# Kernel optimization log

Measured on AMD Instinct MI355X. Metric: run time of the kernel, lower is better.

## Reference

```python
import math
import jax, jax.numpy as jnp
import numpy as np

F, B, J, D, H = 120, 64, 22, 512, 4  # frames, batch, joints, d_model, heads
DFF = 2048
EPS = 1e-6


def setup_inputs() -> dict:
    key = jax.random.key(0)
    ks = jax.random.split(key, 32)
    w = lambda k, s: jax.random.normal(k, s, jnp.float32) * 0.02
    inp = {
        "x": jax.random.normal(ks[0], (F, B, J, D), jnp.float32),
        "timesteps_embs": jax.random.normal(ks[1], (1, B, D), jnp.float32),
        "spat_mask": jnp.ones((1, 1, 1, 1, 1), jnp.int32),
        "temp_mask": jnp.ones((1, 1, 1, 1, 1), jnp.int32),
        "layer_ind": 1,
    }
    i = 2
    for p in ("s", "t"):  # spatial / temporal attention params
        for m in ("q", "k", "v", "o"):
            inp[p + "W" + m] = w(ks[i], (D, D)); i += 1
            inp[p + "b" + m] = w(ks[i], (D,)); i += 1
    inp["ffW1"] = w(ks[i], (D, DFF)); inp["ffb1"] = w(ks[i + 1], (DFF,))
    inp["ffW2"] = w(ks[i + 2], (DFF, D)); inp["ffb2"] = w(ks[i + 3], (D,))
    for n in ("n1", "n2", "n3"):
        inp[n + "a"] = jnp.ones((D,), jnp.float32)
        inp[n + "b"] = jnp.zeros((D,), jnp.float32)
    return inp


def _norm(x, a, b):
    # custom Norm: uses torch.std (ddof=1) and eps added to std (not var)
    mu = jnp.mean(x, axis=-1, keepdims=True)
    sd = jnp.std(x, axis=-1, ddof=1, keepdims=True)
    return a * (x - mu) / (sd + EPS) + b


def _mha(x, Wq, bq, Wk, bk, Wv, bv, Wo, bo, h, mask):
    d1, bs, d2, dm = x.shape
    dk = dm // h
    split = lambda t: (t.reshape(d1, bs, d2, h, dk)).transpose(0, 1, 3, 2, 4)  # (d1,bs,h,d2,dk)
    q = split(x @ Wq + bq)
    k = split(x @ Wk + bk)
    v = split(x @ Wv + bv)
    scores = jnp.einsum("fbhqd,fbhkd->fbhqk", q, k) / math.sqrt(dk)
    m = jnp.swapaxes(mask, 0, 1).astype(jnp.float32)  # mask.transpose(0,1).float()
    scores = jnp.where(m == 0, -1e9, scores)
    p = jax.nn.softmax(scores, axis=-1)
    o = jnp.einsum("fbhqk,fbhkd->fbhqd", p, v)
    o = o.transpose(0, 1, 3, 2, 4).reshape(d1, bs, d2, dm)
    return o @ Wo + bo


def _forward(x, timesteps_embs,
             sWq, sbq, sWk, sbk, sWv, sbv, sWo, sbo,
             tWq, tbq, tWk, tbk, tWv, tbv, tWo, tbo,
             ffW1, ffb1, ffW2, ffb2,
             n1a, n1b, n2a, n2b, n3a, n3b,
             spat_mask, temp_mask):
    # layer_ind > 0 path: no positional-encoding additions (eval mode: dropout = identity)
    f, bs, nj, dm = x.shape
    ts = jnp.broadcast_to(timesteps_embs[:, :, None, :], (f, bs, 1, dm))
    x1 = jnp.concatenate([ts, x], axis=2)                      # (F,B,J+1,D)
    x1 = x + _mha(x1, sWq, sbq, sWk, sbk, sWv, sbv, sWo, sbo, H, spat_mask)[:, :, 1:, :]
    x1 = jnp.swapaxes(_norm(x1, n1a, n1b), 0, 2)               # (J,B,F,D)
    ts2 = jnp.broadcast_to(timesteps_embs[:, :, None, :], (x1.shape[0], bs, 1, dm))
    x2 = jnp.concatenate([ts2, x1], axis=2)                    # (J,B,F+1,D)
    x2 = x1 + _mha(x2, tWq, tbq, tWk, tbk, tWv, tbv, tWo, tbo, H, temp_mask)[:, :, 1:, :]
    x2 = jnp.swapaxes(_norm(x2, n2a, n2b), 0, 2)               # (F,B,J,D)
    ff = jax.nn.gelu(x2 @ ffW1 + ffb1, approximate=False) @ ffW2 + ffb2
    return _norm(x2 + ff, n3a, n3b)


def reference(x, timesteps_embs,
              sWq, sbq, sWk, sbk, sWv, sbv, sWo, sbo,
              tWq, tbq, tWk, tbk, tWv, tbv, tWo, tbo,
              ffW1, ffb1, ffW2, ffb2,
              n1a, n1b, n2a, n2b, n3a, n3b,
              spat_mask, temp_mask, layer_ind):
    # layer_ind is fixed to 1 (layer_ind==0 branch is unreachable/broken in source)
    return _forward(x, timesteps_embs,
                    sWq, sbq, sWk, sbk, sWv, sbv, sWo, sbo,
                    tWq, tbq, tWk, tbk, tWv, tbv, tWo, tbo,
                    ffW1, ffb1, ffW2, ffb2,
                    n1a, n1b, n2a, n2b, n3a, n3b,
                    spat_mask, temp_mask)
```

## Files before the change

kernel.cpp:

```cpp
#include <hip/hip_runtime.h>
#include <hip/hip_bf16.h>
#include <math.h>


#define F_DIM 120
#define B_DIM 64
#define J_DIM 22
#define H_DIM 4
#define M_TOK (F_DIM * B_DIM * J_DIM)

#define DEV static __device__ __forceinline__

typedef short bf16x8 __attribute__((ext_vector_type(8)));
typedef short us8 __attribute__((ext_vector_type(8)));
typedef float f32x4 __attribute__((ext_vector_type(4)));

struct __align__(8) us4 { unsigned short x, y, z, w; };

DEV unsigned short f2b(float f) {
  unsigned u = __float_as_uint(f);
  u += 0x7fffu + ((u >> 16) & 1u);
  return (unsigned short)(u >> 16);
}
DEV float b2f(unsigned short u) { return __uint_as_float(((unsigned)u) << 16); }

#define GLOAD16(g, l)                                                          \
  __builtin_amdgcn_global_load_lds(                                            \
      (const __attribute__((address_space(1))) void*)(g),                      \
      (__attribute__((address_space(3))) void*)(l), 16, 0, 0)

enum { EPI_QKV = 0, EPI_GELU = 1, EPI_RES = 2, EPI_ACC = 3, EPI_RESB = 4,
       EPI_ROB = 5,
       EPI_RBB = 6 };

__global__ __launch_bounds__(256)
void cast_k(const float* __restrict__ in, unsigned short* __restrict__ out, int n8) {
  for (int i = blockIdx.x * 256 + threadIdx.x; i < n8; i += gridDim.x * 256) {
    const float4 a = ((const float4*)in)[i * 2];
    const float4 b = ((const float4*)in)[i * 2 + 1];
    us8 v;
    v[0] = f2b(a.x); v[1] = f2b(a.y); v[2] = f2b(a.z); v[3] = f2b(a.w);
    v[4] = f2b(b.x); v[5] = f2b(b.y); v[6] = f2b(b.z); v[7] = f2b(b.w);
    *(us8*)&out[i * 8] = v;
  }
}

__global__ __launch_bounds__(256)
void tcast_k(const float* __restrict__ W, unsigned short* __restrict__ WT, int K, int N) {
  __shared__ float t[32][33];
  const int n0 = blockIdx.x * 32, k0 = blockIdx.y * 32;
  const int tx = threadIdx.x, ty = threadIdx.y;
#pragma unroll
  for (int i = 0; i < 4; ++i)
    t[ty + i * 8][tx] = W[(size_t)(k0 + ty + i * 8) * N + n0 + tx];
  __syncthreads();
#pragma unroll
  for (int i = 0; i < 4; ++i)
    WT[(size_t)(n0 + ty + i * 8) * K + k0 + tx] = f2b(t[tx][ty + i * 8]);
}

__global__ __launch_bounds__(256)
void tsproj_k(const float* __restrict__ ts, const float* __restrict__ W,
              const float* __restrict__ bias, unsigned short* __restrict__ out) {
  __shared__ float tsr[512];
  const int b = blockIdx.x, tid = threadIdx.x;
  for (int i = tid; i < 512; i += 256) tsr[i] = ts[b * 512 + i];
  __syncthreads();
  const int n0 = tid, n1 = tid + 256;
  float a0 = bias[n0], a1 = bias[n1];
  for (int k = 0; k < 512; ++k) {
    const float t = tsr[k];
    a0 += t * W[(size_t)k * 512 + n0];
    a1 += t * W[(size_t)k * 512 + n1];
  }
  out[b * 512 + n0] = f2b(a0);
  out[b * 512 + n1] = f2b(a1);
}

template<int EPI>
DEV void epi_store(float v, int row, int col, const float* b0, const float* b1,
                   const float* b2, const void* res, float* outF,
                   unsigned short* o0, unsigned short* o1, unsigned short* o2,
                   int ldo, float scale) {
  if constexpr (EPI == EPI_QKV) {
    const int seg = col >> 9;
    const int cl = col & 511;
    const float* bs = (seg == 0) ? b0 : (seg == 1) ? b1 : b2;
    unsigned short* ob = (seg == 0) ? o0 : (seg == 1) ? o1 : o2;
    const float sc = (seg == 0) ? scale : 1.f;
    v = (v + bs[cl]) * sc;
    ob[(size_t)row * 512 + cl] = f2b(v);
  } else if constexpr (EPI == EPI_GELU) {
    v += b0[col];
    const float a2 = 1.5957691216057308f * (v + 0.044715f * v * v * v);
    const float g = v / (1.f + __expf(-a2));
    o0[(size_t)row * ldo + col] = f2b(g);
  } else if constexpr (EPI == EPI_RES) {
    const size_t off = (size_t)row * 512 + col;
    outF[off] = v + b0[col] + ((const float*)res)[off];
  } else if constexpr (EPI == EPI_RESB) {
    const size_t off = (size_t)row * 512 + col;
    outF[off] = v + b0[col] + b2f(((const unsigned short*)res)[off]);
  } else if constexpr (EPI == EPI_ROB) {
    const size_t off = (size_t)row * 512 + col;
    o0[off] = f2b(v + b0[col] + ((const float*)res)[off]);
  } else if constexpr (EPI == EPI_RBB) {
    const size_t off = (size_t)row * 512 + col;
    o0[off] = f2b(v + b0[col] + b2f(((const unsigned short*)res)[off]));
  } else {
    const size_t off = (size_t)row * 512 + col;
    outF[off] = v + outF[off];
  }
}

template<int EPI>
__global__ __launch_bounds__(512, 4)
void gemm256_k(const unsigned short* __restrict__ Ab, const unsigned short* __restrict__ Wt,
               const float* __restrict__ b0, const float* __restrict__ b1, const float* __restrict__ b2,
               const void* __restrict__ res, float* __restrict__ outF,
               unsigned short* __restrict__ o0, unsigned short* __restrict__ o1, unsigned short* __restrict__ o2,
               int lda, int ldw, int ldo, int nk, int nx, float scale) {
  __shared__ unsigned short As[3][8192];
  __shared__ unsigned short Bs[3][4096];
  const int tid = threadIdx.x;
  const int chunkg = gridDim.x >> 3;
  const int wg = (blockIdx.x & 7) * chunkg + (blockIdx.x >> 3);
  const int nbase = (wg % nx) * 128;
  const int mbase = (wg / nx) * 256;
  const int lane = tid & 63;
  const int w = tid >> 6;
  const int wr = (w >> 1) * 64;
  const int wc = (w & 1) * 64;
  const int l15 = lane & 15;
  const int lhi = lane >> 4;

  const int crow = lane >> 2;
  const int ccol = (((lane & 3) ^ ((lane >> 3) & 3)) << 3);
  const unsigned short* gA0 = Ab + (size_t)(mbase + 32 * w + crow) * lda + ccol;
  const unsigned short* gA1 = gA0 + (size_t)16 * lda;
  const unsigned short* gB0 = Wt + (size_t)(nbase + 16 * w + crow) * ldw + ccol;

  auto stage = [&](int bb, int kt) {
    GLOAD16(gA0 + kt, &As[bb][(2 * w) * 512]);
    GLOAD16(gA1 + kt, &As[bb][(2 * w + 1) * 512]);
    GLOAD16(gB0 + kt, &Bs[bb][w * 512]);
  };

  f32x4 acc[4][4] = {};
  const int KT = nk >> 5;
  const int swz = ((lhi ^ ((l15 >> 1) & 3)) << 3);

  stage(0, 0);
  stage(1, 32);
  asm volatile("s_waitcnt vmcnt(3)" ::: "memory");
  __builtin_amdgcn_s_barrier();

  for (int t = 0; t < KT; ++t) {
    const unsigned short* as = As[t % 3];
    const unsigned short* bs = Bs[t % 3];
    if (t + 2 < KT) stage((t + 2) % 3, (t + 2) << 5);
    bf16x8 afr[4], bfr[4];
#pragma unroll
    for (int i = 0; i < 4; ++i) afr[i] = *(const bf16x8*)&as[(wr + i * 16 + l15) * 32 + swz];
#pragma unroll
    for (int j = 0; j < 4; ++j) bfr[j] = *(const bf16x8*)&bs[(wc + j * 16 + l15) * 32 + swz];
#pragma unroll
    for (int i = 0; i < 4; ++i)
#pragma unroll
      for (int j = 0; j < 4; ++j)
        acc[i][j] = __builtin_amdgcn_mfma_f32_16x16x32_bf16(afr[i], bfr[j], acc[i][j], 0, 0, 0);
    if (t + 2 < KT)      asm volatile("s_waitcnt vmcnt(3) lgkmcnt(0)" ::: "memory");
    else if (t + 1 < KT) asm volatile("s_waitcnt vmcnt(0) lgkmcnt(0)" ::: "memory");
    else                 asm volatile("s_waitcnt lgkmcnt(0)" ::: "memory");
    __builtin_amdgcn_s_barrier();
  }

#pragma unroll
  for (int i = 0; i < 4; ++i)
#pragma unroll
    for (int j = 0; j < 4; ++j) {
      const int row0 = mbase + wr + i * 16 + (lhi << 2);
      const int col = nbase + wc + j * 16 + l15;
#pragma unroll
      for (int q = 0; q < 4; ++q)
        epi_store<EPI>(acc[i][j][q], row0 + q, col, b0, b1, b2, res, outF, o0, o1, o2, ldo, scale);
    }
}

template<int EPI>
__global__ __launch_bounds__(256)
void gemm_k(const unsigned short* __restrict__ Ab, const unsigned short* __restrict__ Wt,
            const float* __restrict__ b0, const float* __restrict__ b1, const float* __restrict__ b2,
            const void* __restrict__ res, float* __restrict__ outF,
            unsigned short* __restrict__ o0, unsigned short* __restrict__ o1, unsigned short* __restrict__ o2,
            int lda, int ldw, int ldo, int nk, int nx, float scale) {
  __shared__ unsigned short As[3][4096];
  __shared__ unsigned short Bs[3][4096];
  const int tid = threadIdx.x;
  const int chunkg = gridDim.x >> 3;
  const int wg = (blockIdx.x & 7) * chunkg + (blockIdx.x >> 3);
  const int nbase = (wg % nx) * 128;
  const int mbase = (wg / nx) * 128;
  const int lane = tid & 63;
  const int w = tid >> 6;
  const int wr = (w >> 1) * 64;
  const int wc = (w & 1) * 64;
  const int l15 = lane & 15;
  const int lhi = lane >> 4;

  const int crow = lane >> 2;
  const int ccol = (((lane & 3) ^ ((lane >> 3) & 3)) << 3);
  const unsigned short* gA0 = Ab + (size_t)(mbase + 32 * w + crow) * lda + ccol;
  const unsigned short* gA1 = gA0 + (size_t)16 * lda;
  const unsigned short* gB0 = Wt + (size_t)(nbase + 32 * w + crow) * ldw + ccol;
  const unsigned short* gB1 = gB0 + (size_t)16 * ldw;

  auto stage = [&](int bb, int kt) {
    GLOAD16(gA0 + kt, &As[bb][(2 * w) * 512]);
    GLOAD16(gA1 + kt, &As[bb][(2 * w + 1) * 512]);
    GLOAD16(gB0 + kt, &Bs[bb][(2 * w) * 512]);
    GLOAD16(gB1 + kt, &Bs[bb][(2 * w + 1) * 512]);
  };

  f32x4 acc[4][4] = {};
  const int KT = nk >> 5;
  const int swz = ((lhi ^ ((l15 >> 1) & 3)) << 3);

  stage(0, 0);
  stage(1, 32);
  asm volatile("s_waitcnt vmcnt(4)" ::: "memory");
  __builtin_amdgcn_s_barrier();

  for (int t = 0; t < KT; ++t) {
    const unsigned short* as = As[t % 3];
    const unsigned short* bs = Bs[t % 3];
    if (t + 2 < KT) stage((t + 2) % 3, (t + 2) << 5);
    bf16x8 afr[4], bfr[4];
#pragma unroll
    for (int i = 0; i < 4; ++i) afr[i] = *(const bf16x8*)&as[(wr + i * 16 + l15) * 32 + swz];
#pragma unroll
    for (int j = 0; j < 4; ++j) bfr[j] = *(const bf16x8*)&bs[(wc + j * 16 + l15) * 32 + swz];
#pragma unroll
    for (int i = 0; i < 4; ++i)
#pragma unroll
      for (int j = 0; j < 4; ++j)
        acc[i][j] = __builtin_amdgcn_mfma_f32_16x16x32_bf16(afr[i], bfr[j], acc[i][j], 0, 0, 0);
    if (t + 2 < KT)      asm volatile("s_waitcnt vmcnt(4) lgkmcnt(0)" ::: "memory");
    else if (t + 1 < KT) asm volatile("s_waitcnt vmcnt(0) lgkmcnt(0)" ::: "memory");
    else                 asm volatile("s_waitcnt lgkmcnt(0)" ::: "memory");
    __builtin_amdgcn_s_barrier();
  }

#pragma unroll
  for (int i = 0; i < 4; ++i)
#pragma unroll
    for (int j = 0; j < 4; ++j) {
      const int row0 = mbase + wr + i * 16 + (lhi << 2);
      const int col = nbase + wc + j * 16 + l15;
#pragma unroll
      for (int q = 0; q < 4; ++q)
        epi_store<EPI>(acc[i][j][q], row0 + q, col, b0, b1, b2, res, outF, o0, o1, o2, ldo, scale);
    }
}

template<int EPI>
__global__ __launch_bounds__(256)
void gemmf_k(const float* __restrict__ Af, const unsigned short* __restrict__ Wt,
             const float* __restrict__ b0, const float* __restrict__ b1, const float* __restrict__ b2,
             const void* __restrict__ res, float* __restrict__ outF,
             unsigned short* __restrict__ o0, unsigned short* __restrict__ o1, unsigned short* __restrict__ o2,
             int lda, int ldw, int ldo, int nk, int nx, float scale) {
  __shared__ unsigned short As[128][40];
  __shared__ unsigned short Bs[128][40];
  const int tid = threadIdx.x;
  const int chunkg = gridDim.x >> 3;
  const int wg = (blockIdx.x & 7) * chunkg + (blockIdx.x >> 3);
  const int nbase = (wg % nx) * 128;
  const int mbase = (wg / nx) * 128;
  const int lane = tid & 63;
  const int w = tid >> 6;
  const int wr = (w >> 1) * 64;
  const int wc = (w & 1) * 64;
  const int l15 = lane & 15;
  const int lhi = lane >> 4;

  float4 ra[4];
  us4 rb[4];
  auto loadAB = [&](int kt) {
#pragma unroll
    for (int i = 0; i < 4; ++i) {
      const int g = i * 256 + tid;
      const int r = g >> 3;
      const int c = (g & 7) << 2;
      ra[i] = *(const float4*)(Af + (size_t)(mbase + r) * lda + kt + c);
      rb[i] = *(const us4*)(Wt + (size_t)(nbase + r) * ldw + kt + c);
    }
  };
  auto storeAB = [&]() {
#pragma unroll
    for (int i = 0; i < 4; ++i) {
      const int g = i * 256 + tid;
      const int r = g >> 3;
      const int c = (g & 7) << 2;
      us4 ua;
      ua.x = f2b(ra[i].x); ua.y = f2b(ra[i].y); ua.z = f2b(ra[i].z); ua.w = f2b(ra[i].w);
      *(us4*)&As[r][c] = ua;
      *(us4*)&Bs[r][c] = rb[i];
    }
  };

  f32x4 acc[4][4] = {};
  const int KT = nk >> 5;
  loadAB(0);
  storeAB();
  __syncthreads();
  for (int t = 0; t < KT; ++t) {
    if (t + 1 < KT) loadAB((t + 1) << 5);
    bf16x8 afr[4], bfr[4];
    const int klo = lhi << 3;
#pragma unroll
    for (int i = 0; i < 4; ++i) afr[i] = *(const bf16x8*)&As[wr + i * 16 + l15][klo];
#pragma unroll
    for (int j = 0; j < 4; ++j) bfr[j] = *(const bf16x8*)&Bs[wc + j * 16 + l15][klo];
#pragma unroll
    for (int i = 0; i < 4; ++i)
#pragma unroll
      for (int j = 0; j < 4; ++j)
        acc[i][j] = __builtin_amdgcn_mfma_f32_16x16x32_bf16(afr[i], bfr[j], acc[i][j], 0, 0, 0);
    __syncthreads();
    if (t + 1 < KT) { storeAB(); __syncthreads(); }
  }

#pragma unroll
  for (int i = 0; i < 4; ++i)
#pragma unroll
    for (int j = 0; j < 4; ++j) {
      const int row0 = mbase + wr + i * 16 + (lhi << 2);
      const int col = nbase + wc + j * 16 + l15;
#pragma unroll
      for (int q = 0; q < 4; ++q)
        epi_store<EPI>(acc[i][j][q], row0 + q, col, b0, b1, b2, res, outF, o0, o1, o2, ldo, scale);
    }
}

__global__ __launch_bounds__(256)
void attn_t_k(const unsigned short* __restrict__ Qb, const unsigned short* __restrict__ Kb,
              const unsigned short* __restrict__ Vb, const unsigned short* __restrict__ kts,
              const unsigned short* __restrict__ vts, unsigned short* __restrict__ Ob) {
  __shared__ unsigned short Ps[128][134];
  __shared__ unsigned short Vt[64][134];
  const int tid = threadIdx.x;
  const int inst = blockIdx.x >> 2;
  const int h = blockIdx.x & 3;
  const int b = inst & (B_DIM - 1);
  const size_t rowbase = (size_t)inst * 120;
  const int hoff = h * 128;
  const int lane = tid & 63;
  const int w = tid >> 6;
  const int wr = w * 32;
  const int l15 = lane & 15;
  const int lhi = lane >> 4;

  auto stageV = [&](int half) {
    for (int e = tid; e < 2048; e += 256) {
      const int d4 = (e & 15) << 2;
      const int key = e >> 4;
      us4 v;
      if (key <= 120) {
        const unsigned short* src = (key == 0) ? (vts + b * 512) : (Vb + (rowbase + key - 1) * 512);
        v = *(const us4*)(src + hoff + half * 64 + d4);
      } else { v.x = 0; v.y = 0; v.z = 0; v.w = 0; }
      Vt[d4 + 0][key] = v.x; Vt[d4 + 1][key] = v.y; Vt[d4 + 2][key] = v.z; Vt[d4 + 3][key] = v.w;
    }
  };
  stageV(0);

  bf16x8 qa[2][4];
#pragma unroll
  for (int i = 0; i < 2; ++i) {
    const int row = min(wr + i * 16 + l15, 119);
    const unsigned short* qp = Qb + (rowbase + row) * 512 + hoff;
#pragma unroll
    for (int kt = 0; kt < 4; ++kt)
      qa[i][kt] = *(const bf16x8*)(qp + kt * 32 + lhi * 8);
  }

  f32x4 acc[2][8] = {};
#pragma unroll
  for (int kt = 0; kt < 4; ++kt) {
    const int klo = kt * 32 + lhi * 8;
    bf16x8 kb[8];
#pragma unroll
    for (int j = 0; j < 8; ++j) {
      const int key = min(j * 16 + l15, 120);
      const unsigned short* kp = (key == 0) ? (kts + b * 512) : (Kb + (rowbase + key - 1) * 512);
      kb[j] = *(const bf16x8*)(kp + hoff + klo);
    }
#pragma unroll
    for (int i = 0; i < 2; ++i)
#pragma unroll
      for (int j = 0; j < 8; ++j)
        acc[i][j] = __builtin_amdgcn_mfma_f32_16x16x32_bf16(qa[i][kt], kb[j], acc[i][j], 0, 0, 0);
  }

  float rinv[2][4];
#pragma unroll
  for (int i = 0; i < 2; ++i)
#pragma unroll
    for (int q = 0; q < 4; ++q) {
      float m = -1e30f;
#pragma unroll
      for (int j = 0; j < 8; ++j)
        if (j * 16 + l15 <= 120) m = fmaxf(m, acc[i][j][q]);
#pragma unroll
      for (int mk = 1; mk < 16; mk <<= 1) m = fmaxf(m, __shfl_xor(m, mk, 64));
      float s = 0.f;
#pragma unroll
      for (int j = 0; j < 8; ++j) {
        const float e = (j * 16 + l15 <= 120) ? __expf(acc[i][j][q] - m) : 0.f;
        acc[i][j][q] = e; s += e;
      }
#pragma unroll
      for (int mk = 1; mk < 16; mk <<= 1) s += __shfl_xor(s, mk, 64);
      rinv[i][q] = 1.f / s;
    }

#pragma unroll
  for (int i = 0; i < 2; ++i)
#pragma unroll
    for (int j = 0; j < 8; ++j)
#pragma unroll
      for (int q = 0; q < 4; ++q)
        Ps[wr + i * 16 + lhi * 4 + q][j * 16 + l15] = f2b(acc[i][j][q]);

  __syncthreads();

#pragma unroll
  for (int half = 0; half < 2; ++half) {
    if (half == 1) {
      __syncthreads();
      stageV(1);
      __syncthreads();
    }
    f32x4 oac[2][4] = {};
#pragma unroll
    for (int kt = 0; kt < 4; ++kt) {
      const int klo = kt * 32 + lhi * 8;
      bf16x8 pa[2], vb[4];
#pragma unroll
      for (int i = 0; i < 2; ++i) pa[i] = *(const bf16x8*)&Ps[wr + i * 16 + l15][klo];
#pragma unroll
      for (int jd = 0; jd < 4; ++jd) vb[jd] = *(const bf16x8*)&Vt[jd * 16 + l15][klo];
#pragma unroll
      for (int i = 0; i < 2; ++i)
#pragma unroll
        for (int jd = 0; jd < 4; ++jd)
          oac[i][jd] = __builtin_amdgcn_mfma_f32_16x16x32_bf16(pa[i], vb[jd], oac[i][jd], 0, 0, 0);
    }
#pragma unroll
    for (int i = 0; i < 2; ++i)
#pragma unroll
      for (int q = 0; q < 4; ++q) {
        const int r = wr + i * 16 + lhi * 4 + q;
        if (r < 120) {
          const float sc = rinv[i][q];
#pragma unroll
          for (int jd = 0; jd < 4; ++jd)
            Ob[(rowbase + r) * 512 + hoff + half * 64 + jd * 16 + l15] = f2b(oac[i][jd][q] * sc);
        }
      }
  }
}

__global__ __launch_bounds__(256)
void attn_s_k(const unsigned short* __restrict__ Qb, const unsigned short* __restrict__ Kb,
              const unsigned short* __restrict__ Vb, const unsigned short* __restrict__ kts,
              const unsigned short* __restrict__ vts, unsigned short* __restrict__ Ob) {
  __shared__ unsigned short Ps[4][32][34];
  __shared__ unsigned short Vt[4][128][34];
  const int tid = threadIdx.x;
  const int inst = blockIdx.x;
  const int b = inst & (B_DIM - 1);
  const size_t rowbase = (size_t)inst * 22;
  const int lane = tid & 63;
  const int h = tid >> 6;
  const int l15 = lane & 15;
  const int lhi = lane >> 4;
  const int hoff = h * 128;

  for (int e = tid; e < 4096; e += 256) {
    const int h2 = e >> 10;
    const int rem = e & 1023;
    const int key = rem >> 5;
    const int d4 = (rem & 31) << 2;
    us4 v;
    if (key <= 22) {
      const unsigned short* src = (key == 0) ? (vts + b * 512) : (Vb + (rowbase + key - 1) * 512);
      v = *(const us4*)(src + h2 * 128 + d4);
    } else { v.x = 0; v.y = 0; v.z = 0; v.w = 0; }
    Vt[h2][d4 + 0][key] = v.x; Vt[h2][d4 + 1][key] = v.y; Vt[h2][d4 + 2][key] = v.z; Vt[h2][d4 + 3][key] = v.w;
  }

  bf16x8 qa[2][4];
#pragma unroll
  for (int i = 0; i < 2; ++i) {
    const int row = min(i * 16 + l15, 21);
    const unsigned short* qp = Qb + (rowbase + row) * 512 + hoff;
#pragma unroll
    for (int kt = 0; kt < 4; ++kt)
      qa[i][kt] = *(const bf16x8*)(qp + kt * 32 + lhi * 8);
  }

  f32x4 acc[2][2] = {};
#pragma unroll
  for (int kt = 0; kt < 4; ++kt) {
    const int klo = kt * 32 + lhi * 8;
    bf16x8 kb[2];
#pragma unroll
    for (int j = 0; j < 2; ++j) {
      const int key = min(j * 16 + l15, 22);
      const unsigned short* kp = (key == 0) ? (kts + b * 512) : (Kb + (rowbase + key - 1) * 512);
      kb[j] = *(const bf16x8*)(kp + hoff + klo);
    }
#pragma unroll
    for (int i = 0; i < 2; ++i)
#pragma unroll
      for (int j = 0; j < 2; ++j)
        acc[i][j] = __builtin_amdgcn_mfma_f32_16x16x32_bf16(qa[i][kt], kb[j], acc[i][j], 0, 0, 0);
  }

  float rinv[2][4];
#pragma unroll
  for (int i = 0; i < 2; ++i)
#pragma unroll
    for (int q = 0; q < 4; ++q) {
      float m = -1e30f;
#pragma unroll
      for (int j = 0; j < 2; ++j)
        if (j * 16 + l15 <= 22) m = fmaxf(m, acc[i][j][q]);
#pragma unroll
      for (int mk = 1; mk < 16; mk <<= 1) m = fmaxf(m, __shfl_xor(m, mk, 64));
      float s = 0.f;
#pragma unroll
      for (int j = 0; j < 2; ++j) {
        const float e = (j * 16 + l15 <= 22) ? __expf(acc[i][j][q] - m) : 0.f;
        acc[i][j][q] = e; s += e;
      }
#pragma unroll
      for (int mk = 1; mk < 16; mk <<= 1) s += __shfl_xor(s, mk, 64);
      rinv[i][q] = 1.f / s;
    }

#pragma unroll
  for (int i = 0; i < 2; ++i)
#pragma unroll
    for (int j = 0; j < 2; ++j)
#pragma unroll
      for (int q = 0; q < 4; ++q)
        Ps[h][i * 16 + lhi * 4 + q][j * 16 + l15] = f2b(acc[i][j][q]);

  __syncthreads();

  f32x4 oac[2][8] = {};
  {
    const int klo = lhi * 8;
    bf16x8 pa[2];
#pragma unroll
    for (int i = 0; i < 2; ++i) pa[i] = *(const bf16x8*)&Ps[h][i * 16 + l15][klo];
#pragma unroll
    for (int jd = 0; jd < 8; ++jd) {
      const bf16x8 vb = *(const bf16x8*)&Vt[h][jd * 16 + l15][klo];
#pragma unroll
      for (int i = 0; i < 2; ++i)
        oac[i][jd] = __builtin_amdgcn_mfma_f32_16x16x32_bf16(pa[i], vb, oac[i][jd], 0, 0, 0);
    }
  }

#pragma unroll
  for (int i = 0; i < 2; ++i)
#pragma unroll
    for (int q = 0; q < 4; ++q) {
      const int r = i * 16 + lhi * 4 + q;
      if (r < 22) {
        const float sc = rinv[i][q];
#pragma unroll
        for (int jd = 0; jd < 8; ++jd)
          Ob[(rowbase + r) * 512 + hoff + jd * 16 + l15] = f2b(oac[i][jd][q] * sc);
      }
    }
}

__global__ __launch_bounds__(256)
void norm_k(const float* __restrict__ in, float* __restrict__ out,
            unsigned short* __restrict__ outB,
            const float* __restrict__ ga, const float* __restrict__ gb, const int mode) {
  const int r = blockIdx.x * 4 + (threadIdx.x >> 6);
  const int lane = threadIdx.x & 63;
  const float* row = in + (size_t)r * 512;
  const float4 v0 = *(const float4*)&row[lane * 4];
  const float4 v1 = *(const float4*)&row[256 + lane * 4];
  float s = v0.x + v0.y + v0.z + v0.w + v1.x + v1.y + v1.z + v1.w;
  float ss = v0.x * v0.x + v0.y * v0.y + v0.z * v0.z + v0.w * v0.w
           + v1.x * v1.x + v1.y * v1.y + v1.z * v1.z + v1.w * v1.w;
#pragma unroll
  for (int m = 1; m < 64; m <<= 1) { s += __shfl_xor(s, m, 64); ss += __shfl_xor(ss, m, 64); }
  const float mean = s * (1.f / 512.f);
  const float var = (ss - 512.f * mean * mean) * (1.f / 511.f);
  const float inv = 1.f / (sqrtf(fmaxf(var, 0.f)) + 1e-6f);
  int ro;
  if (mode == 0) ro = r;
  else if (mode == 1) {
    const int f = r / (B_DIM * J_DIM);
    const int bb = (r / J_DIM) % B_DIM;
    const int j = r % J_DIM;
    ro = (j * B_DIM + bb) * F_DIM + f;
  } else {
    const int j = r / (B_DIM * F_DIM);
    const int bb = (r / F_DIM) % B_DIM;
    const int f = r % F_DIM;
    ro = (f * B_DIM + bb) * J_DIM + j;
  }
  const float4 g0 = *(const float4*)&ga[lane * 4];
  const float4 g1 = *(const float4*)&ga[256 + lane * 4];
  const float4 h0 = *(const float4*)&gb[lane * 4];
  const float4 h1 = *(const float4*)&gb[256 + lane * 4];
  float4 y0, y1;
  y0.x = g0.x * (v0.x - mean) * inv + h0.x;
  y0.y = g0.y * (v0.y - mean) * inv + h0.y;
  y0.z = g0.z * (v0.z - mean) * inv + h0.z;
  y0.w = g0.w * (v0.w - mean) * inv + h0.w;
  y1.x = g1.x * (v1.x - mean) * inv + h1.x;
  y1.y = g1.y * (v1.y - mean) * inv + h1.y;
  y1.z = g1.z * (v1.z - mean) * inv + h1.z;
  y1.w = g1.w * (v1.w - mean) * inv + h1.w;
  if (out) {
    float* orow = out + (size_t)ro * 512;
    *(float4*)&orow[lane * 4] = y0;
    *(float4*)&orow[256 + lane * 4] = y1;
  }
  if (outB) {
    us4 a, b;
    a.x = f2b(y0.x); a.y = f2b(y0.y); a.z = f2b(y0.z); a.w = f2b(y0.w);
    b.x = f2b(y1.x); b.y = f2b(y1.y); b.z = f2b(y1.z); b.w = f2b(y1.w);
    *(us4*)&outB[(size_t)ro * 512 + lane * 4] = a;
    *(us4*)&outB[(size_t)ro * 512 + 256 + lane * 4] = b;
  }
}

__global__ __launch_bounds__(256)
void normb_k(const unsigned short* __restrict__ in, float* __restrict__ out,
             unsigned short* __restrict__ outB,
             const float* __restrict__ ga, const float* __restrict__ gb, const int mode) {
  const int r = blockIdx.x * 4 + (threadIdx.x >> 6);
  const int lane = threadIdx.x & 63;
  const us8 wv = *(const us8*)&in[(size_t)r * 512 + lane * 8];
  float v[8];
  float s = 0.f, ss = 0.f;
#pragma unroll
  for (int e = 0; e < 8; ++e) {
    v[e] = b2f((unsigned short)wv[e]);
    s += v[e]; ss += v[e] * v[e];
  }
#pragma unroll
  for (int m = 1; m < 64; m <<= 1) { s += __shfl_xor(s, m, 64); ss += __shfl_xor(ss, m, 64); }
  const float mean = s * (1.f / 512.f);
  const float var = (ss - 512.f * mean * mean) * (1.f / 511.f);
  const float inv = 1.f / (sqrtf(fmaxf(var, 0.f)) + 1e-6f);
  int ro;
  if (mode == 0) ro = r;
  else if (mode == 1) {
    const int f = r / (B_DIM * J_DIM);
    const int bb = (r / J_DIM) % B_DIM;
    const int j = r % J_DIM;
    ro = (j * B_DIM + bb) * F_DIM + f;
  } else {
    const int j = r / (B_DIM * F_DIM);
    const int bb = (r / F_DIM) % B_DIM;
    const int f = r % F_DIM;
    ro = (f * B_DIM + bb) * J_DIM + j;
  }
  const float4 g0 = *(const float4*)&ga[lane * 8];
  const float4 g1 = *(const float4*)&ga[lane * 8 + 4];
  const float4 h0 = *(const float4*)&gb[lane * 8];
  const float4 h1 = *(const float4*)&gb[lane * 8 + 4];
  float y[8];
  y[0] = g0.x * (v[0] - mean) * inv + h0.x;
  y[1] = g0.y * (v[1] - mean) * inv + h0.y;
  y[2] = g0.z * (v[2] - mean) * inv + h0.z;
  y[3] = g0.w * (v[3] - mean) * inv + h0.w;
  y[4] = g1.x * (v[4] - mean) * inv + h1.x;
  y[5] = g1.y * (v[5] - mean) * inv + h1.y;
  y[6] = g1.z * (v[6] - mean) * inv + h1.z;
  y[7] = g1.w * (v[7] - mean) * inv + h1.w;
  if (out) {
    float* orow = out + (size_t)ro * 512 + lane * 8;
    *(float4*)&orow[0] = *(float4*)&y[0];
    *(float4*)&orow[4] = *(float4*)&y[4];
  }
  if (outB) {
    us8 o;
#pragma unroll
    for (int e = 0; e < 8; ++e) o[e] = f2b(y[e]);
    *(us8*)&outB[(size_t)ro * 512 + lane * 8] = o;
  }
}

extern "C" void kernel_launch(void* const* d_in, const int* in_sizes, int n_in,
                              void* d_out, int out_size, void* d_ws, size_t ws_size,
                              hipStream_t stream) {
  const float* x   = (const float*)d_in[0];
  const float* tse = (const float*)d_in[1];
  const float* sWq = (const float*)d_in[5];  const float* sbq = (const float*)d_in[6];
  const float* sWk = (const float*)d_in[7];  const float* sbk = (const float*)d_in[8];
  const float* sWv = (const float*)d_in[9];  const float* sbv = (const float*)d_in[10];
  const float* sWo = (const float*)d_in[11]; const float* sbo = (const float*)d_in[12];
  const float* tWq = (const float*)d_in[13]; const float* tbq = (const float*)d_in[14];
  const float* tWk = (const float*)d_in[15]; const float* tbk = (const float*)d_in[16];
  const float* tWv = (const float*)d_in[17]; const float* tbv = (const float*)d_in[18];
  const float* tWo = (const float*)d_in[19]; const float* tbo = (const float*)d_in[20];
  const float* ffW1 = (const float*)d_in[21]; const float* ffb1 = (const float*)d_in[22];
  const float* ffW2 = (const float*)d_in[23]; const float* ffb2 = (const float*)d_in[24];
  const float* n1a = (const float*)d_in[25]; const float* n1b = (const float*)d_in[26];
  const float* n2a = (const float*)d_in[27]; const float* n2b = (const float*)d_in[28];
  const float* n3a = (const float*)d_in[29]; const float* n3b = (const float*)d_in[30];

  char* p = (char*)d_ws;
  auto carve = [&](size_t bytes) { void* r = (void*)p; p += (bytes + 255) & ~(size_t)255; return r; };

  unsigned short* sQKVt = (unsigned short*)carve((size_t)3 * 512 * 512 * 2);
  unsigned short* sOT   = (unsigned short*)carve((size_t)512 * 512 * 2);
  unsigned short* tQKVt = (unsigned short*)carve((size_t)3 * 512 * 512 * 2);
  unsigned short* tOT   = (unsigned short*)carve((size_t)512 * 512 * 2);
  unsigned short* W1T   = (unsigned short*)carve((size_t)2048 * 512 * 2);
  unsigned short* W2T   = (unsigned short*)carve((size_t)512 * 2048 * 2);
  unsigned short* ktss  = (unsigned short*)carve((size_t)64 * 512 * 2);
  unsigned short* vtss  = (unsigned short*)carve((size_t)64 * 512 * 2);
  unsigned short* ktst  = (unsigned short*)carve((size_t)64 * 512 * 2);
  unsigned short* vtst  = (unsigned short*)carve((size_t)64 * 512 * 2);
  unsigned short* Qb    = (unsigned short*)carve((size_t)M_TOK * 512 * 2);

  unsigned short* Kb = (unsigned short*)d_out;
  unsigned short* Vb = Kb + (size_t)M_TOK * 512;
  float* outF = (float*)d_out;

  const bool bigws = ws_size >= (size_t)873725952ull;
  float* Rbuf = nullptr;
  unsigned short* Hb  = nullptr;
  unsigned short* xb  = nullptr;
  unsigned short* rb1 = nullptr;
  if (bigws) {
    Hb = (unsigned short*)carve((size_t)M_TOK * 2048 * 2);
    xb = Hb;
    rb1 = Hb + (size_t)M_TOK * 512;
  } else {
    Rbuf = (float*)carve((size_t)M_TOK * 512 * 4);
  }

  const float QSCALE = 0.08838834764831845f;

  {
    dim3 tb(32, 8);
    tcast_k<<<dim3(16, 16), tb, 0, stream>>>(sWq, sQKVt, 512, 512);
    tcast_k<<<dim3(16, 16), tb, 0, stream>>>(sWk, sQKVt + 262144, 512, 512);
    tcast_k<<<dim3(16, 16), tb, 0, stream>>>(sWv, sQKVt + 524288, 512, 512);
    tcast_k<<<dim3(16, 16), tb, 0, stream>>>(sWo, sOT, 512, 512);
    tcast_k<<<dim3(16, 16), tb, 0, stream>>>(tWq, tQKVt, 512, 512);
    tcast_k<<<dim3(16, 16), tb, 0, stream>>>(tWk, tQKVt + 262144, 512, 512);
    tcast_k<<<dim3(16, 16), tb, 0, stream>>>(tWv, tQKVt + 524288, 512, 512);
    tcast_k<<<dim3(16, 16), tb, 0, stream>>>(tWo, tOT, 512, 512);
    tcast_k<<<dim3(64, 16), tb, 0, stream>>>(ffW1, W1T, 512, 2048);
    tcast_k<<<dim3(16, 64), tb, 0, stream>>>(ffW2, W2T, 2048, 512);
  }
  tsproj_k<<<B_DIM, 256, 0, stream>>>(tse, sWk, sbk, ktss);
  tsproj_k<<<B_DIM, 256, 0, stream>>>(tse, sWv, sbv, vtss);
  tsproj_k<<<B_DIM, 256, 0, stream>>>(tse, tWk, tbk, ktst);
  tsproj_k<<<B_DIM, 256, 0, stream>>>(tse, tWv, tbv, vtst);

  const int MT = M_TOK / 128;
  const int MT2 = M_TOK / 256;

  if (bigws) {
    cast_k<<<2048, 256, 0, stream>>>(x, xb, M_TOK * 512 / 8);
    gemm256_k<EPI_QKV><<<12 * MT2, 512, 0, stream>>>(
        xb, sQKVt, sbq, sbk, sbv, nullptr, nullptr, Qb, Kb, Vb, 512, 512, 512, 512, 12, QSCALE);
    attn_s_k<<<dim3(F_DIM * B_DIM), 256, 0, stream>>>(Qb, Kb, Vb, ktss, vtss, Qb);
    gemm256_k<EPI_ROB><<<4 * MT2, 512, 0, stream>>>(
        Qb, sOT, sbo, nullptr, nullptr, x, nullptr, Kb, nullptr, nullptr, 512, 512, 512, 512, 4, 1.f);
    normb_k<<<M_TOK / 4, 256, 0, stream>>>(Kb, nullptr, rb1, n1a, n1b, 1);

    gemm256_k<EPI_QKV><<<12 * MT2, 512, 0, stream>>>(
        rb1, tQKVt, tbq, tbk, tbv, nullptr, nullptr, Qb, Kb, Vb, 512, 512, 512, 512, 12, QSCALE);
    attn_t_k<<<dim3(J_DIM * B_DIM * H_DIM), 256, 0, stream>>>(Qb, Kb, Vb, ktst, vtst, Qb);
    gemm256_k<EPI_RBB><<<4 * MT2, 512, 0, stream>>>(
        Qb, tOT, tbo, nullptr, nullptr, rb1, nullptr, Kb, nullptr, nullptr, 512, 512, 512, 512, 4, 1.f);
    normb_k<<<M_TOK / 4, 256, 0, stream>>>(Kb, nullptr, Qb, n2a, n2b, 2);

    gemm256_k<EPI_GELU><<<16 * MT2, 512, 0, stream>>>(
        Qb, W1T, ffb1, nullptr, nullptr, nullptr, nullptr, Hb, nullptr, nullptr,
        512, 512, 2048, 512, 16, 1.f);
    gemm256_k<EPI_RBB><<<4 * MT2, 512, 0, stream>>>(
        Hb, W2T, ffb2, nullptr, nullptr, Qb, nullptr, Qb, nullptr, nullptr,
        2048, 2048, 512, 2048, 4, 1.f);
    normb_k<<<M_TOK / 4, 256, 0, stream>>>(Qb, outF, nullptr, n3a, n3b, 0);
  } else {
    gemmf_k<EPI_QKV><<<12 * MT, 256, 0, stream>>>(
        x, sQKVt, sbq, sbk, sbv, nullptr, nullptr, Qb, Kb, Vb, 512, 512, 512, 512, 12, QSCALE);
    attn_s_k<<<dim3(F_DIM * B_DIM), 256, 0, stream>>>(Qb, Kb, Vb, ktss, vtss, Qb);
    gemm_k<EPI_RES><<<4 * MT, 256, 0, stream>>>(
        Qb, sOT, sbo, nullptr, nullptr, x, outF, nullptr, nullptr, nullptr, 512, 512, 512, 512, 4, 1.f);
    norm_k<<<M_TOK / 4, 256, 0, stream>>>(outF, Rbuf, nullptr, n1a, n1b, 1);

    gemmf_k<EPI_QKV><<<12 * MT, 256, 0, stream>>>(
        Rbuf, tQKVt, tbq, tbk, tbv, nullptr, nullptr, Qb, Kb, Vb, 512, 512, 512, 512, 12, QSCALE);
    attn_t_k<<<dim3(J_DIM * B_DIM * H_DIM), 256, 0, stream>>>(Qb, Kb, Vb, ktst, vtst, Qb);
    gemm_k<EPI_RES><<<4 * MT, 256, 0, stream>>>(
        Qb, tOT, tbo, nullptr, nullptr, Rbuf, outF, nullptr, nullptr, nullptr, 512, 512, 512, 512, 4, 1.f);
    norm_k<<<M_TOK / 4, 256, 0, stream>>>(outF, Rbuf, Qb, n2a, n2b, 2);

    for (int c = 0; c < 4; ++c) {
      gemm_k<EPI_GELU><<<4 * MT, 256, 0, stream>>>(
          Qb, W1T + (size_t)c * 512 * 512, ffb1 + c * 512, nullptr, nullptr,
          nullptr, nullptr, Qb, nullptr, nullptr, 512, 512, 512, 512, 4, 1.f);
      if (c == 0)
        gemm_k<EPI_RES><<<4 * MT, 256, 0, stream>>>(
            Qb, W2T + c * 512, ffb2, nullptr, nullptr, Rbuf, outF,
            nullptr, nullptr, nullptr, 512, 2048, 512, 512, 4, 1.f);
      else
        gemm_k<EPI_ACC><<<4 * MT, 256, 0, stream>>>(
            Qb, W2T + c * 512, nullptr, nullptr, nullptr, nullptr, outF,
            nullptr, nullptr, nullptr, 512, 2048, 512, 512, 4, 1.f);
    }
    norm_k<<<M_TOK / 4, 256, 0, stream>>>(outF, outF, nullptr, n3a, n3b, 0);
  }
}
```

Baseline: 3.210 ms.

## Batch weight casts and ts projections into single launches; read bf16 residual

Merges the eight 512x512 weight transpose-cast launches into one 3D-grid kernel and the four timestep projection launches into one kernel. The projection kernel now splits K across four thread groups with a shared-memory reduction, giving it more parallelism. The spatial output-projection epilogue now reads the residual from the bf16 copy of x instead of the fp32 input, which cuts residual read bandwidth but rounds the residual to bf16. These setup kernels are small next to the GEMMs, so the overall effect is likely small.

```diff
diff --git a/kernel.cpp b/kernel.cpp
--- a/kernel.cpp
+++ b/kernel.cpp
@@ -59,22 +59,47 @@
     WT[(size_t)(n0 + ty + i * 8) * K + k0 + tx] = f2b(t[tx][ty + i * 8]);
 }
 
+struct Tc8Args { const float* W[8]; unsigned short* WT[8]; };
 __global__ __launch_bounds__(256)
-void tsproj_k(const float* __restrict__ ts, const float* __restrict__ W,
-              const float* __restrict__ bias, unsigned short* __restrict__ out) {
+void tcast8_k(Tc8Args a) {
+  __shared__ float t[32][33];
+  const float* W = a.W[blockIdx.z];
+  unsigned short* WT = a.WT[blockIdx.z];
+  const int n0 = blockIdx.x * 32, k0 = blockIdx.y * 32;
+  const int tx = threadIdx.x, ty = threadIdx.y;
+#pragma unroll
+  for (int i = 0; i < 4; ++i)
+    t[ty + i * 8][tx] = W[(size_t)(k0 + ty + i * 8) * 512 + n0 + tx];
+  __syncthreads();
+#pragma unroll
+  for (int i = 0; i < 4; ++i)
+    WT[(size_t)(n0 + ty + i * 8) * 512 + k0 + tx] = f2b(t[tx][ty + i * 8]);
+}
+
+struct TsArgs { const float* W[4]; const float* bias[4]; unsigned short* out[4]; };
+__global__ __launch_bounds__(1024)
+void tsproj_k(const float* __restrict__ ts, TsArgs a) {
   __shared__ float tsr[512];
-  const int b = blockIdx.x, tid = threadIdx.x;
-  for (int i = tid; i < 512; i += 256) tsr[i] = ts[b * 512 + i];
+  __shared__ float red[3][256];
+  const int b = blockIdx.x;
+  const int nb = blockIdx.y;
+  const int pj = blockIdx.z;
+  const int t = threadIdx.x;
+  const int n = nb * 256 + (t & 255);
+  const int kh = t >> 8;
+  if (t < 512) tsr[t] = ts[b * 512 + t];
   __syncthreads();
-  const int n0 = tid, n1 = tid + 256;
-  float a0 = bias[n0], a1 = bias[n1];
-  for (int k = 0; k < 512; ++k) {
-    const float t = tsr[k];
-    a0 += t * W[(size_t)k * 512 + n0];
-    a1 += t * W[(size_t)k * 512 + n1];
-  }
-  out[b * 512 + n0] = f2b(a0);
-  out[b * 512 + n1] = f2b(a1);
+  const float* W = a.W[pj];
+  float acc = 0.f;
+  const int k0 = kh * 128;
+  for (int k = k0; k < k0 + 128; ++k)
+    acc += tsr[k] * W[(size_t)k * 512 + n];
+  if (kh) red[kh - 1][t & 255] = acc;
+  __syncthreads();
+  if (kh == 0) {
+    acc += red[0][t & 255] + red[1][t & 255] + red[2][t & 255];
+    a.out[pj][b * 512 + n] = f2b(acc + a.bias[pj][n]);
+  }
 }
 
 template<int EPI>
@@ -760,21 +785,27 @@
 
   {
     dim3 tb(32, 8);
-    tcast_k<<<dim3(16, 16), tb, 0, stream>>>(sWq, sQKVt, 512, 512);
-    tcast_k<<<dim3(16, 16), tb, 0, stream>>>(sWk, sQKVt + 262144, 512, 512);
-    tcast_k<<<dim3(16, 16), tb, 0, stream>>>(sWv, sQKVt + 524288, 512, 512);
-    tcast_k<<<dim3(16, 16), tb, 0, stream>>>(sWo, sOT, 512, 512);
-    tcast_k<<<dim3(16, 16), tb, 0, stream>>>(tWq, tQKVt, 512, 512);
-    tcast_k<<<dim3(16, 16), tb, 0, stream>>>(tWk, tQKVt + 262144, 512, 512);
-    tcast_k<<<dim3(16, 16), tb, 0, stream>>>(tWv, tQKVt + 524288, 512, 512);
-    tcast_k<<<dim3(16, 16), tb, 0, stream>>>(tWo, tOT, 512, 512);
+    Tc8Args tc;
+    tc.W[0] = sWq; tc.WT[0] = sQKVt;
+    tc.W[1] = sWk; tc.WT[1] = sQKVt + 262144;
+    tc.W[2] = sWv; tc.WT[2] = sQKVt + 524288;
+    tc.W[3] = sWo; tc.WT[3] = sOT;
+    tc.W[4] = tWq; tc.WT[4] = tQKVt;
+    tc.W[5] = tWk; tc.WT[5] = tQKVt + 262144;
+    tc.W[6] = tWv; tc.WT[6] = tQKVt + 524288;
+    tc.W[7] = tWo; tc.WT[7] = tOT;
+    tcast8_k<<<dim3(16, 16, 8), tb, 0, stream>>>(tc);
     tcast_k<<<dim3(64, 16), tb, 0, stream>>>(ffW1, W1T, 512, 2048);
     tcast_k<<<dim3(16, 64), tb, 0, stream>>>(ffW2, W2T, 2048, 512);
   }
-  tsproj_k<<<B_DIM, 256, 0, stream>>>(tse, sWk, sbk, ktss);
-  tsproj_k<<<B_DIM, 256, 0, stream>>>(tse, sWv, sbv, vtss);
-  tsproj_k<<<B_DIM, 256, 0, stream>>>(tse, tWk, tbk, ktst);
-  tsproj_k<<<B_DIM, 256, 0, stream>>>(tse, tWv, tbv, vtst);
+  {
+    TsArgs ta;
+    ta.W[0] = sWk; ta.bias[0] = sbk; ta.out[0] = ktss;
+    ta.W[1] = sWv; ta.bias[1] = sbv; ta.out[1] = vtss;
+    ta.W[2] = tWk; ta.bias[2] = tbk; ta.out[2] = ktst;
+    ta.W[3] = tWv; ta.bias[3] = tbv; ta.out[3] = vtst;
+    tsproj_k<<<dim3(B_DIM, 2, 4), 1024, 0, stream>>>(tse, ta);
+  }
 
   const int MT = M_TOK / 128;
   const int MT2 = M_TOK / 256;
@@ -784,8 +815,8 @@
     gemm256_k<EPI_QKV><<<12 * MT2, 512, 0, stream>>>(
         xb, sQKVt, sbq, sbk, sbv, nullptr, nullptr, Qb, Kb, Vb, 512, 512, 512, 512, 12, QSCALE);
     attn_s_k<<<dim3(F_DIM * B_DIM), 256, 0, stream>>>(Qb, Kb, Vb, ktss, vtss, Qb);
-    gemm256_k<EPI_ROB><<<4 * MT2, 512, 0, stream>>>(
-        Qb, sOT, sbo, nullptr, nullptr, x, nullptr, Kb, nullptr, nullptr, 512, 512, 512, 512, 4, 1.f);
+    gemm256_k<EPI_RBB><<<4 * MT2, 512, 0, stream>>>(
+        Qb, sOT, sbo, nullptr, nullptr, xb, nullptr, Kb, nullptr, nullptr, 512, 512, 512, 512, 4, 1.f);
     normb_k<<<M_TOK / 4, 256, 0, stream>>>(Kb, nullptr, rb1, n1a, n1b, 1);
 
     gemm256_k<EPI_QKV><<<12 * MT2, 512, 0, stream>>>(
```

New measurement: 3.085 ms. -3.9%, faster.
